# Kernel optimization log

Hardware: AMD Instinct MI355X
Metric: run time of the kernel (lower is better)

## Reference

```python
import jax, jax.numpy as jnp
import numpy as np
import math

B, S, E, R = 128, 16, 512, 500  # batch, seq_len, emb_size, relation_num


def setup_inputs() -> dict:
    key = jax.random.key(0)
    ks = jax.random.split(key, 12)
    s = 1.0 / math.sqrt(E)
    emb = jax.random.normal(ks[0], (R + 1, E), jnp.float32) * s
    emb = emb.at[R].set(0.0)  # padding_idx row is zero in torch
    w_ih = jax.random.normal(ks[1], (4 * E, E), jnp.float32) * s
    w_hh = jax.random.normal(ks[2], (4 * E, E), jnp.float32) * s
    b_ih = jax.random.normal(ks[3], (4 * E,), jnp.float32) * s
    b_hh = jax.random.normal(ks[4], (4 * E,), jnp.float32) * s
    fc_w = jax.random.normal(ks[5], (1, E), jnp.float32) * s
    fc_b = jax.random.normal(ks[6], (1,), jnp.float32) * s
    fcq_w = jax.random.normal(ks[7], (E, E), jnp.float32) * s
    fcq_b = jax.random.normal(ks[8], (E,), jnp.float32) * s
    fck_w = jax.random.normal(ks[9], (E, E), jnp.float32) * s
    fck_b = jax.random.normal(ks[10], (E,), jnp.float32) * s
    tokens = jax.random.randint(ks[11], (B, S), 0, R)  # avoid padding idx R
    return dict(tokens=tokens, emb=emb, w_ih=w_ih, w_hh=w_hh, b_ih=b_ih,
                b_hh=b_hh, fc_w=fc_w, fc_b=fc_b, fcq_w=fcq_w, fcq_b=fcq_b,
                fck_w=fck_w, fck_b=fck_b)


def _lstm_pair(x, w_ih, w_hh, b):
    # x: [..., 2, E]; 2-step LSTM from zero state, return final hidden [..., E]
    def cell(xt, h, c):
        g = xt @ w_ih.T + h @ w_hh.T + b
        i, f, gg, o = jnp.split(g, 4, axis=-1)  # torch gate order i,f,g,o
        c = jax.nn.sigmoid(f) * c + jax.nn.sigmoid(i) * jnp.tanh(gg)
        return jax.nn.sigmoid(o) * jnp.tanh(c), c
    z = jnp.zeros_like(x[..., 0, :])
    h1, c1 = cell(x[..., 0, :], z, z)
    h2, _ = cell(x[..., 1, :], h1, c1)
    return h2


def _attention(x, rel_emb, fcq_w, fcq_b, fck_w, fck_b):
    # x: [B,q,E]; keys = [relation embeddings ; x] -> scores [B,q,R+q]
    b = x.shape[0]
    rel = jnp.broadcast_to(rel_emb[None], (b,) + rel_emb.shape)
    kin = jnp.concatenate([rel, x], axis=1)
    k = kin @ fck_w.T + fck_b
    q = x @ fcq_w.T + fcq_b
    return jnp.einsum('bqe,bke->bqk', q, k) / math.sqrt(E)


def _entropy(scores):
    lp = jax.nn.log_softmax(scores, axis=-1)
    return -jnp.sum(jnp.exp(lp) * lp, axis=-1)


def reference(tokens, emb, w_ih, w_hh, b_ih, b_hh, fc_w, fc_b,
              fcq_w, fcq_b, fck_w, fck_b):
    b_lstm = b_ih + b_hh
    rel_emb = emb[:R]  # relation embeddings used as attention keys/values
    cur = emb[tokens]  # [B,S,E]
    bidx = jnp.arange(B)
    losses = []
    for L in range(S, 1, -1):  # lengths processed: S, S-1, ..., 2
        if L > 2:
            # all adjacent pairs, batched 2-step LSTM: [B, L-1, E]
            pairs = jnp.stack([cur[:, :-1], cur[:, 1:]], axis=2)
            h = _lstm_pair(pairs, w_ih, w_hh, b_lstm)
            sc = jax.nn.sigmoid(h @ fc_w.T + fc_b)[..., 0]  # [B, L-1]
            sel = jnp.argmax(sc, axis=-1)  # [B]
            selected = jnp.take_along_axis(h, sel[:, None, None], axis=1)  # [B,1,E]
            scores = _attention(selected, rel_emb, fcq_w, fcq_b, fck_w, fck_b)
            losses.append(_entropy(scores))  # [B,1]
            # weightedAverage: mask is all-False for seq_len==1, plain softmax
            prob = jax.nn.softmax(scores, axis=-1)  # [B,1,R+1]
            all_emb = jnp.concatenate(
                [jnp.broadcast_to(rel_emb[None], (B, R, E)), selected], axis=1)
            merged = jnp.einsum('bqk,bke->bqe', prob, all_emb)[:, 0]  # [B,E]
            # output = inputs.detach().clone(); write merged at sel; drop row sel+1
            base = jax.lax.stop_gradient(cur)
            base = base.at[bidx, sel].set(merged)
            j = jnp.arange(L - 1)[None, :]
            src = j + (j > sel[:, None]).astype(j.dtype)
            cur = jnp.take_along_axis(base, src[:, :, None], axis=1)  # [B,L-1,E]
        else:  # L == 2: plain LSTM over the two tokens
            h = _lstm_pair(cur, w_ih, w_hh, b_lstm)  # [B,E]
            cur = h[:, None, :]
            losses.append(jnp.zeros((B, 1), cur.dtype))
    scores_f = _attention(cur, rel_emb, fcq_w, fcq_b, fck_w, fck_b)  # [B,1,R+1]
    losses.append(_entropy(scores_f))
    loss_tensor = jnp.concatenate(losses, axis=-1)  # [B,S]
    return scores_f[:, 0], loss_tensor
```

## Files before the change

### kernel.cpp

```cpp
#include <hip/hip_runtime.h>
#include <hip/hip_bf16.h>

#define BB 128
#define SS 16
#define EE 512
#define RR 500
#define G4 2048
#define OUT0 64128
#define NSC 501
#define NPAIR 2047
#define NSU 1012

__device__ __forceinline__ float sigm(float x) { return 1.f / (1.f + expf(-x)); }

__device__ float g_blstm[G4];
__device__ float g_blstmr[G4];
__device__ float g_wihr[G4 * EE];
__device__ float g_whhr[G4 * EE];
__device__ float g_fcw[EE + 4];
__device__ float g_qbias[1024];
__device__ float g_Krel[RR * EE];
__device__ float g_cur[BB * SS * EE];
__device__ float g_G[BB * SS * G4];
__device__ float g_h1[BB * SS * EE];
__device__ float g_c1[BB * SS * EE];
__device__ float g_h2[BB * SS * EE];
__device__ float g_sc[BB * SS];
__device__ float g_ent[BB * SS];
__device__ int   g_sel[BB];
__device__ int   g_ord[BB * SS];
__device__ float g_fckwT[EE * EE];
__device__ float g_fcqwT[EE * EE];
__device__ float g_W2[RR * EE];
__device__ float g_Mx[EE * EE];
__device__ float g_c2[RR + 4];
__device__ float g_v1[EE];
__device__ float g_c0[1];
__device__ float g_su[BB * NSU];

__global__ void k_prep(const float* __restrict__ bih, const float* __restrict__ bhh,
                       const float* __restrict__ fcwv, const float* __restrict__ fcbv,
                       const float* __restrict__ fcqb, const float* __restrict__ fckb) {
    int i = blockIdx.x * blockDim.x + threadIdx.x;
    if (i < G4) g_blstm[i] = bih[i] + bhh[i];
    if (i < EE) {
        g_fcw[i] = fcwv[i];
        g_qbias[i] = fcqb[i];
        g_qbias[EE + i] = fckb[i];
    }
    if (i == 0) g_fcw[EE] = fcbv[0];
    if (i < BB * SS) g_ord[i] = i;
}

__global__ void k_reord(const float* __restrict__ wih, const float* __restrict__ whh) {
    int i = blockIdx.x * blockDim.x + threadIdx.x;
    if (i >= G4 * EE) return;
    int n = i >> 9;
    int k = i & (EE - 1);
    int e = n & (EE - 1);
    int gate = n >> 9;
    int np = 4 * e + gate;
    g_wihr[(size_t)np * EE + k] = wih[i];
    g_whhr[(size_t)np * EE + k] = whh[i];
    if (k == 0) g_blstmr[np] = g_blstm[n];
}

__global__ void k_gather(const int* __restrict__ tok, const float* __restrict__ emb) {
    int i = blockIdx.x * blockDim.x + threadIdx.x;
    if (i >= BB * SS * EE) return;
    int e = i & (EE - 1);
    int r = i >> 9;
    int t = tok[r];
    g_cur[i] = emb[(size_t)t * EE + e];
}

__global__ void k_tr(const float* __restrict__ fckw, const float* __restrict__ fcqw) {
    int i = blockIdx.x * blockDim.x + threadIdx.x;
    if (i >= EE * EE) return;
    int ep = i >> 9;
    int f = i & (EE - 1);
    g_fckwT[(size_t)f * EE + ep] = fckw[(size_t)ep * EE + f];
    g_fcqwT[(size_t)f * EE + ep] = fcqw[(size_t)ep * EE + f];
}

__global__ __launch_bounds__(512) void k_vprep(const float* __restrict__ fcqw, const float* __restrict__ fckw) {
    __shared__ float sh[512];
    int t = threadIdx.x;
    int blk = blockIdx.x;
    if (blk == 0) {
        float acc = 0.f;
        for (int ep = 0; ep < EE; ep++)
            acc += g_qbias[ep] * fckw[(size_t)ep * EE + t] + g_qbias[EE + ep] * fcqw[(size_t)ep * EE + t];
        g_v1[t] = acc;
    } else if (blk == 1) {
        sh[t] = g_qbias[t] * g_qbias[EE + t];
        __syncthreads();
        for (int s = 256; s > 0; s >>= 1) { if (t < s) sh[t] += sh[t + s]; __syncthreads(); }
        if (t == 0) g_c0[0] = sh[0];
    } else {
        int k = blk - 2;
        sh[t] = g_Krel[(size_t)k * EE + t] * g_qbias[t];
        __syncthreads();
        for (int s = 256; s > 0; s >>= 1) { if (t < s) sh[t] += sh[t + s]; __syncthreads(); }
        if (t == 0) g_c2[k] = sh[0];
    }
}

#define TM 32
#define TN 64
#define TK 32
__device__ __forceinline__ void gemm_dev(
    const float* __restrict__ A, int lda,
    const float* __restrict__ W, int ldw,
    const float* __restrict__ bias, const float* __restrict__ Dadd, int ldd,
    float* __restrict__ C, int ldc, int M, int N, int K)
{
    __shared__ __align__(16) float As[2][TK][TM + 2];
    __shared__ __align__(16) float Ws[2][TK][TN + 4];
    int tid = threadIdx.x;
    int mt = blockIdx.y * TM;
    int nt = blockIdx.x * TN;
    int tr = tid >> 4;
    int tc = tid & 15;
    float acc[2][4] = {{0.f,0.f,0.f,0.f},{0.f,0.f,0.f,0.f}};

    int ea = tid * 4;
    int ra = ea >> 5;
    int ka = ea & 31;
    int gmA = mt + ra;
    bool rokA = gmA < M;
    const float* Arow = A + (size_t)(rokA ? gmA : 0) * lda;
    int ew = tid * 8;
    int rw = ew >> 5;
    int kw = ew & 31;
    int gnW = nt + rw;
    bool rokW = gnW < N;
    const float* Wrow = W + (size_t)(rokW ? gnW : 0) * ldw;

    float4 pa = {0,0,0,0}, pw0 = {0,0,0,0}, pw1 = {0,0,0,0};
    if (rokA) pa = *(const float4*)&Arow[ka];
    if (rokW) { pw0 = *(const float4*)&Wrow[kw]; pw1 = *(const float4*)&Wrow[kw + 4]; }
    As[0][ka + 0][ra] = pa.x; As[0][ka + 1][ra] = pa.y; As[0][ka + 2][ra] = pa.z; As[0][ka + 3][ra] = pa.w;
    Ws[0][kw + 0][rw] = pw0.x; Ws[0][kw + 1][rw] = pw0.y; Ws[0][kw + 2][rw] = pw0.z; Ws[0][kw + 3][rw] = pw0.w;
    Ws[0][kw + 4][rw] = pw1.x; Ws[0][kw + 5][rw] = pw1.y; Ws[0][kw + 6][rw] = pw1.z; Ws[0][kw + 7][rw] = pw1.w;
    __syncthreads();

    int P = K / TK;
    for (int p = 0; p < P; p++) {
        int cur = p & 1;
        bool more = (p + 1) < P;
        if (more) {
            int k2 = (p + 1) * TK;
            if (rokA) pa = *(const float4*)&Arow[k2 + ka];
            if (rokW) { pw0 = *(const float4*)&Wrow[k2 + kw]; pw1 = *(const float4*)&Wrow[k2 + kw + 4]; }
        }
        #pragma unroll
        for (int kk = 0; kk < TK; kk++) {
            const float2 a = *(const float2*)&As[cur][kk][2 * tr];
            const float4 w = *(const float4*)&Ws[cur][kk][4 * tc];
            acc[0][0] += a.x * w.x; acc[0][1] += a.x * w.y; acc[0][2] += a.x * w.z; acc[0][3] += a.x * w.w;
            acc[1][0] += a.y * w.x; acc[1][1] += a.y * w.y; acc[1][2] += a.y * w.z; acc[1][3] += a.y * w.w;
        }
        if (more) {
            int nxt = cur ^ 1;
            As[nxt][ka + 0][ra] = pa.x; As[nxt][ka + 1][ra] = pa.y; As[nxt][ka + 2][ra] = pa.z; As[nxt][ka + 3][ra] = pa.w;
            Ws[nxt][kw + 0][rw] = pw0.x; Ws[nxt][kw + 1][rw] = pw0.y; Ws[nxt][kw + 2][rw] = pw0.z; Ws[nxt][kw + 3][rw] = pw0.w;
            Ws[nxt][kw + 4][rw] = pw1.x; Ws[nxt][kw + 5][rw] = pw1.y; Ws[nxt][kw + 6][rw] = pw1.z; Ws[nxt][kw + 7][rw] = pw1.w;
        }
        __syncthreads();
    }
    #pragma unroll
    for (int i = 0; i < 2; i++) {
        int gm = mt + 2 * tr + i;
        if (gm >= M) continue;
        #pragma unroll
        for (int j = 0; j < 4; j++) {
            int gn = nt + 4 * tc + j;
            if (gn >= N) continue;
            float v = (i == 0) ? ((j == 0) ? acc[0][0] : (j == 1) ? acc[0][1] : (j == 2) ? acc[0][2] : acc[0][3])
                               : ((j == 0) ? acc[1][0] : (j == 1) ? acc[1][1] : (j == 2) ? acc[1][2] : acc[1][3]);
            if (bias) v += bias[gn];
            if (Dadd) v += Dadd[(size_t)gm * ldd + gn];
            C[(size_t)gm * ldc + gn] = v;
        }
    }
}

#define UM 128
#define UN 64
#define UK 32
template<int MODE>
__global__ __launch_bounds__(256) void kg_bigF() {
    __shared__ __align__(16) float As[UK][UM + 4];
    __shared__ __align__(16) float Ws[UK][UN + 4];
    const float* __restrict__ A = (MODE == 0) ? g_cur : g_h1;
    const float* __restrict__ W = (MODE == 0) ? g_wihr : g_whhr;
    const int M = (MODE == 0) ? (BB * SS) : NPAIR;
    int tid = threadIdx.x;
    int mt = blockIdx.y * UM;
    int nt = blockIdx.x * UN;
    int tr = tid >> 4;
    int tc = tid & 15;
    float acc[8][4] = {};

    int ra = tid & 127;
    int ka = (tid >> 7) << 4;
    int gmA = mt + ra;
    bool rokA = gmA < M;
    const float* Arow = A + (size_t)(rokA ? gmA : 0) * EE;
    int rw = tid & 63;
    int kw = (tid >> 6) << 3;
    const float* Wrow = W + (size_t)(nt + rw) * EE;

    float4 pa[4] = {};
    float4 pw[2];
    #pragma unroll
    for (int j = 0; j < 4; j++) if (rokA) pa[j] = *(const float4*)&Arow[ka + 4 * j];
    #pragma unroll
    for (int j = 0; j < 2; j++) pw[j] = *(const float4*)&Wrow[kw + 4 * j];

    for (int kt = 0; kt < EE; kt += UK) {
        #pragma unroll
        for (int j = 0; j < 4; j++) {
            As[ka + 4 * j + 0][ra] = pa[j].x;
            As[ka + 4 * j + 1][ra] = pa[j].y;
            As[ka + 4 * j + 2][ra] = pa[j].z;
            As[ka + 4 * j + 3][ra] = pa[j].w;
        }
        #pragma unroll
        for (int j = 0; j < 2; j++) {
            Ws[kw + 4 * j + 0][rw] = pw[j].x;
            Ws[kw + 4 * j + 1][rw] = pw[j].y;
            Ws[kw + 4 * j + 2][rw] = pw[j].z;
            Ws[kw + 4 * j + 3][rw] = pw[j].w;
        }
        __syncthreads();
        if (kt + UK < EE) {
            int k2 = kt + UK;
            #pragma unroll
            for (int j = 0; j < 4; j++) if (rokA) pa[j] = *(const float4*)&Arow[k2 + ka + 4 * j];
            #pragma unroll
            for (int j = 0; j < 2; j++) pw[j] = *(const float4*)&Wrow[k2 + kw + 4 * j];
        }
        #pragma unroll
        for (int kk = 0; kk < UK; kk++) {
            const float4 aA = *(const float4*)&As[kk][4 * tr];
            const float4 aB = *(const float4*)&As[kk][64 + 4 * tr];
            const float4 w4 = *(const float4*)&Ws[kk][4 * tc];
            const float am[8] = {aA.x, aA.y, aA.z, aA.w, aB.x, aB.y, aB.z, aB.w};
            const float wn[4] = {w4.x, w4.y, w4.z, w4.w};
            #pragma unroll
            for (int i = 0; i < 8; i++)
                #pragma unroll
                for (int j = 0; j < 4; j++)
                    acc[i][j] += am[i] * wn[j];
        }
        __syncthreads();
    }

    int c0 = nt + 4 * tc;
    int e0 = (nt >> 2) + tc;
    #pragma unroll
    for (int ri = 0; ri < 8; ri++) {
        int row = (ri < 4) ? (4 * tr + ri) : (60 + 4 * tr + ri);
        int gm = mt + row;
        if (gm >= M) continue;
        float qx = acc[ri][0], qy = acc[ri][1], qz = acc[ri][2], qw = acc[ri][3];
        if (MODE == 0) {
            const float4 b4 = *(const float4*)&g_blstmr[c0];
            qx += b4.x; qy += b4.y; qz += b4.z; qw += b4.w;
            float4 o = {qx, qy, qz, qw};
            *(float4*)&g_G[(size_t)gm * G4 + c0] = o;
            float cA = sigm(qx) * tanhf(qz);
            g_c1[(size_t)gm * EE + e0] = cA;
            g_h1[(size_t)gm * EE + e0] = sigm(qw) * tanhf(cA);
        } else {
            const float4 d4 = *(const float4*)&g_G[(size_t)(gm + 1) * G4 + c0];
            qx += d4.x; qy += d4.y; qz += d4.z; qw += d4.w;
            float c1v = g_c1[(size_t)gm * EE + e0];
            float cA = sigm(qy) * c1v + sigm(qx) * tanhf(qz);
            g_h2[(size_t)gm * EE + e0] = sigm(qw) * tanhf(cA);
        }
    }
}

__global__ __launch_bounds__(256) void kg_Krel(const float* __restrict__ emb, const float* __restrict__ fckw) {
    gemm_dev(emb, EE, fckw, EE, g_qbias + EE, nullptr, 0, g_Krel, EE, RR, EE, EE);
}
__global__ __launch_bounds__(256) void kg_W2() {
    gemm_dev(g_Krel, EE, g_fcqwT, EE, nullptr, nullptr, 0, g_W2, EE, RR, EE, EE);
}
__global__ __launch_bounds__(256) void kg_Mx() {
    gemm_dev(g_fckwT, EE, g_fcqwT, EE, nullptr, nullptr, 0, g_Mx, EE, EE, EE, EE);
}

__global__ __launch_bounds__(256) void k_scI() {
    int m = blockIdx.x;
    int t = threadIdx.x;
    __shared__ float red[256];
    const float* h = g_h2 + (size_t)m * EE;
    float part = h[t] * g_fcw[t] + h[t + 256] * g_fcw[t + 256];
    red[t] = part;
    __syncthreads();
    for (int s = 128; s > 0; s >>= 1) { if (t < s) red[t] += red[t + s]; __syncthreads(); }
    if (t == 0) g_sc[m] = red[0];
}

__global__ __launch_bounds__(256) void k_scP(int L) {
    int m = blockIdx.x;
    int b = m >> 1;
    int tcand = m & 1;
    int s = g_sel[b];
    int p = s - 1 + tcand;
    bool valid = tcand == 0 ? (s >= 1) : (s <= L - 3);
    if (!valid) return;
    int physL = g_ord[b * SS + p];
    int t = threadIdx.x;
    __shared__ float red[256];
    const float* h = g_h2 + (size_t)physL * EE;
    float part = h[t] * g_fcw[t] + h[t + 256] * g_fcw[t + 256];
    red[t] = part;
    __syncthreads();
    for (int s2 = 128; s2 > 0; s2 >>= 1) { if (t < s2) red[t] += red[t + s2]; __syncthreads(); }
    if (t == 0) g_sc[b * SS + p] = red[0];
}

__global__ __launch_bounds__(256) void kg_su(int P) {
    __shared__ __align__(16) float As[2][TK][TM + 2];
    __shared__ __align__(16) float Ws[2][TK][TN + 4];
    __shared__ int s_phys[TM];
    int tid = threadIdx.x;
    int mt = blockIdx.y * TM;
    int nt = blockIdx.x * TN;
    int tr = tid >> 4;
    int tc = tid & 15;
    float acc[2][4] = {{0.f,0.f,0.f,0.f},{0.f,0.f,0.f,0.f}};

    if (tid < TM) {
        int b = mt + tid;
        float best = -1e30f; int bi = 0;
        for (int p = 0; p < P; p++) {
            float v = g_sc[b * SS + p];
            if (v > best) { best = v; bi = p; }
        }
        s_phys[tid] = g_ord[b * SS + bi];
        if (blockIdx.x == 0) g_sel[b] = bi;
    }
    __syncthreads();

    int ea = tid * 4;
    int ra = ea >> 5;
    int ka = ea & 31;
    const float* Arow = g_h2 + (size_t)s_phys[ra] * EE;
    int ew = tid * 8;
    int rw = ew >> 5;
    int kw = ew & 31;
    int gnW = nt + rw;
    bool rokW = gnW < NSU;
    const float* Wrow = nullptr;
    if (rokW) Wrow = (gnW < RR) ? (g_W2 + (size_t)gnW * EE) : (g_Mx + (size_t)(gnW - RR) * EE);

    float4 pa = *(const float4*)&Arow[ka];
    float4 pw0 = {0,0,0,0}, pw1 = {0,0,0,0};
    if (rokW) { pw0 = *(const float4*)&Wrow[kw]; pw1 = *(const float4*)&Wrow[kw + 4]; }
    As[0][ka + 0][ra] = pa.x; As[0][ka + 1][ra] = pa.y; As[0][ka + 2][ra] = pa.z; As[0][ka + 3][ra] = pa.w;
    Ws[0][kw + 0][rw] = pw0.x; Ws[0][kw + 1][rw] = pw0.y; Ws[0][kw + 2][rw] = pw0.z; Ws[0][kw + 3][rw] = pw0.w;
    Ws[0][kw + 4][rw] = pw1.x; Ws[0][kw + 5][rw] = pw1.y; Ws[0][kw + 6][rw] = pw1.z; Ws[0][kw + 7][rw] = pw1.w;
    __syncthreads();

    const int NP = EE / TK;
    for (int p = 0; p < NP; p++) {
        int cur = p & 1;
        bool more = (p + 1) < NP;
        if (more) {
            int k2 = (p + 1) * TK;
            pa = *(const float4*)&Arow[k2 + ka];
            if (rokW) { pw0 = *(const float4*)&Wrow[k2 + kw]; pw1 = *(const float4*)&Wrow[k2 + kw + 4]; }
        }
        #pragma unroll
        for (int kk = 0; kk < TK; kk++) {
            const float2 a = *(const float2*)&As[cur][kk][2 * tr];
            const float4 w = *(const float4*)&Ws[cur][kk][4 * tc];
            acc[0][0] += a.x * w.x; acc[0][1] += a.x * w.y; acc[0][2] += a.x * w.z; acc[0][3] += a.x * w.w;
            acc[1][0] += a.y * w.x; acc[1][1] += a.y * w.y; acc[1][2] += a.y * w.z; acc[1][3] += a.y * w.w;
        }
        if (more) {
            int nxt = cur ^ 1;
            As[nxt][ka + 0][ra] = pa.x; As[nxt][ka + 1][ra] = pa.y; As[nxt][ka + 2][ra] = pa.z; As[nxt][ka + 3][ra] = pa.w;
            Ws[nxt][kw + 0][rw] = pw0.x; Ws[nxt][kw + 1][rw] = pw0.y; Ws[nxt][kw + 2][rw] = pw0.z; Ws[nxt][kw + 3][rw] = pw0.w;
            Ws[nxt][kw + 4][rw] = pw1.x; Ws[nxt][kw + 5][rw] = pw1.y; Ws[nxt][kw + 6][rw] = pw1.z; Ws[nxt][kw + 7][rw] = pw1.w;
        }
        __syncthreads();
    }
    #pragma unroll
    for (int i = 0; i < 2; i++) {
        int gm = mt + 2 * tr + i;
        #pragma unroll
        for (int j = 0; j < 4; j++) {
            int gn = nt + 4 * tc + j;
            if (gn >= NSU) continue;
            float v = (i == 0) ? ((j == 0) ? acc[0][0] : (j == 1) ? acc[0][1] : (j == 2) ? acc[0][2] : acc[0][3])
                               : ((j == 0) ? acc[1][0] : (j == 1) ? acc[1][1] : (j == 2) ? acc[1][2] : acc[1][3]);
            g_su[(size_t)gm * NSU + gn] = v + (gn < RR ? g_c2[gn] : 0.f);
        }
    }
}

__global__ __launch_bounds__(256) void kg_GiF() {
    __shared__ __align__(16) float As[2][TK][TM + 2];
    __shared__ __align__(16) float Ws[2][TK][TN + 4];
    __shared__ int s_phys[TM];
    int tid = threadIdx.x;
    int mt = blockIdx.y * TM;
    int nt = blockIdx.x * TN;
    int tr = tid >> 4;
    int tc = tid & 15;
    float acc[2][4] = {{0.f,0.f,0.f,0.f},{0.f,0.f,0.f,0.f}};

    if (tid < TM) {
        int b = mt + tid;
        s_phys[tid] = g_ord[b * SS + g_sel[b]];
    }
    __syncthreads();

    int ea = tid * 4;
    int ra = ea >> 5;
    int ka = ea & 31;
    const float* Arow = g_cur + (size_t)s_phys[ra] * EE;
    int ew = tid * 8;
    int rw = ew >> 5;
    int kw = ew & 31;
    const float* Wrow = g_wihr + (size_t)(nt + rw) * EE;

    float4 pa = *(const float4*)&Arow[ka];
    float4 pw0 = *(const float4*)&Wrow[kw];
    float4 pw1 = *(const float4*)&Wrow[kw + 4];
    As[0][ka + 0][ra] = pa.x; As[0][ka + 1][ra] = pa.y; As[0][ka + 2][ra] = pa.z; As[0][ka + 3][ra] = pa.w;
    Ws[0][kw + 0][rw] = pw0.x; Ws[0][kw + 1][rw] = pw0.y; Ws[0][kw + 2][rw] = pw0.z; Ws[0][kw + 3][rw] = pw0.w;
    Ws[0][kw + 4][rw] = pw1.x; Ws[0][kw + 5][rw] = pw1.y; Ws[0][kw + 6][rw] = pw1.z; Ws[0][kw + 7][rw] = pw1.w;
    __syncthreads();

    const int NP = EE / TK;
    for (int p = 0; p < NP; p++) {
        int cur = p & 1;
        bool more = (p + 1) < NP;
        if (more) {
            int k2 = (p + 1) * TK;
            pa = *(const float4*)&Arow[k2 + ka];
            pw0 = *(const float4*)&Wrow[k2 + kw];
            pw1 = *(const float4*)&Wrow[k2 + kw + 4];
        }
        #pragma unroll
        for (int kk = 0; kk < TK; kk++) {
            const float2 a = *(const float2*)&As[cur][kk][2 * tr];
            const float4 w = *(const float4*)&Ws[cur][kk][4 * tc];
            acc[0][0] += a.x * w.x; acc[0][1] += a.x * w.y; acc[0][2] += a.x * w.z; acc[0][3] += a.x * w.w;
            acc[1][0] += a.y * w.x; acc[1][1] += a.y * w.y; acc[1][2] += a.y * w.z; acc[1][3] += a.y * w.w;
        }
        if (more) {
            int nxt = cur ^ 1;
            As[nxt][ka + 0][ra] = pa.x; As[nxt][ka + 1][ra] = pa.y; As[nxt][ka + 2][ra] = pa.z; As[nxt][ka + 3][ra] = pa.w;
            Ws[nxt][kw + 0][rw] = pw0.x; Ws[nxt][kw + 1][rw] = pw0.y; Ws[nxt][kw + 2][rw] = pw0.z; Ws[nxt][kw + 3][rw] = pw0.w;
            Ws[nxt][kw + 4][rw] = pw1.x; Ws[nxt][kw + 5][rw] = pw1.y; Ws[nxt][kw + 6][rw] = pw1.z; Ws[nxt][kw + 7][rw] = pw1.w;
        }
        __syncthreads();
    }
    int c0 = nt + 4 * tc;
    int e0 = (nt >> 2) + tc;
    const float4 b4 = *(const float4*)&g_blstmr[c0];
    #pragma unroll
    for (int i = 0; i < 2; i++) {
        int phys = s_phys[2 * tr + i];
        float qx = acc[i][0] + b4.x;
        float qy = acc[i][1] + b4.y;
        float qz = acc[i][2] + b4.z;
        float qw = acc[i][3] + b4.w;
        float4 o = {qx, qy, qz, qw};
        *(float4*)&g_G[(size_t)phys * G4 + c0] = o;
        float cA = sigm(qx) * tanhf(qz);
        g_c1[(size_t)phys * EE + e0] = cA;
        g_h1[(size_t)phys * EE + e0] = sigm(qw) * tanhf(cA);
    }
}

__global__ __launch_bounds__(256) void kg_g2iF(int L) {
    __shared__ __align__(16) float As[2][TK][TM + 2];
    __shared__ __align__(16) float Ws[2][TK][TN + 4];
    __shared__ int s_physA[TM];
    __shared__ int s_physD[TM];
    __shared__ int s_val[TM];
    int tid = threadIdx.x;
    int mt = blockIdx.y * TM;
    int nt = blockIdx.x * TN;
    int tr = tid >> 4;
    int tc = tid & 15;
    float acc[2][4] = {{0.f,0.f,0.f,0.f},{0.f,0.f,0.f,0.f}};

    if (tid < TM) {
        int gm = mt + tid;
        int b = gm >> 1;
        int tcand = gm & 1;
        int s = g_sel[b];
        int p = min(max(s - 1 + tcand, 0), 14);
        s_physA[tid] = g_ord[b * SS + p];
        s_physD[tid] = g_ord[b * SS + p + 1];
        s_val[tid] = tcand == 0 ? (s >= 1) : (s <= L - 3);
    }
    __syncthreads();

    int ea = tid * 4;
    int ra = ea >> 5;
    int ka = ea & 31;
    const float* Arow = g_h1 + (size_t)s_physA[ra] * EE;
    int ew = tid * 8;
    int rw = ew >> 5;
    int kw = ew & 31;
    const float* Wrow = g_whhr + (size_t)(nt + rw) * EE;

    float4 pa = *(const float4*)&Arow[ka];
    float4 pw0 = *(const float4*)&Wrow[kw];
    float4 pw1 = *(const float4*)&Wrow[kw + 4];
    As[0][ka + 0][ra] = pa.x; As[0][ka + 1][ra] = pa.y; As[0][ka + 2][ra] = pa.z; As[0][ka + 3][ra] = pa.w;
    Ws[0][kw + 0][rw] = pw0.x; Ws[0][kw + 1][rw] = pw0.y; Ws[0][kw + 2][rw] = pw0.z; Ws[0][kw + 3][rw] = pw0.w;
    Ws[0][kw + 4][rw] = pw1.x; Ws[0][kw + 5][rw] = pw1.y; Ws[0][kw + 6][rw] = pw1.z; Ws[0][kw + 7][rw] = pw1.w;
    __syncthreads();

    const int NP = EE / TK;
    for (int p = 0; p < NP; p++) {
        int cur = p & 1;
        bool more = (p + 1) < NP;
        if (more) {
            int k2 = (p + 1) * TK;
            pa = *(const float4*)&Arow[k2 + ka];
            pw0 = *(const float4*)&Wrow[k2 + kw];
            pw1 = *(const float4*)&Wrow[k2 + kw + 4];
        }
        #pragma unroll
        for (int kk = 0; kk < TK; kk++) {
            const float2 a = *(const float2*)&As[cur][kk][2 * tr];
            const float4 w = *(const float4*)&Ws[cur][kk][4 * tc];
            acc[0][0] += a.x * w.x; acc[0][1] += a.x * w.y; acc[0][2] += a.x * w.z; acc[0][3] += a.x * w.w;
            acc[1][0] += a.y * w.x; acc[1][1] += a.y * w.y; acc[1][2] += a.y * w.z; acc[1][3] += a.y * w.w;
        }
        if (more) {
            int nxt = cur ^ 1;
            As[nxt][ka + 0][ra] = pa.x; As[nxt][ka + 1][ra] = pa.y; As[nxt][ka + 2][ra] = pa.z; As[nxt][ka + 3][ra] = pa.w;
            Ws[nxt][kw + 0][rw] = pw0.x; Ws[nxt][kw + 1][rw] = pw0.y; Ws[nxt][kw + 2][rw] = pw0.z; Ws[nxt][kw + 3][rw] = pw0.w;
            Ws[nxt][kw + 4][rw] = pw1.x; Ws[nxt][kw + 5][rw] = pw1.y; Ws[nxt][kw + 6][rw] = pw1.z; Ws[nxt][kw + 7][rw] = pw1.w;
        }
        __syncthreads();
    }
    int c0 = nt + 4 * tc;
    int e0 = (nt >> 2) + tc;
    #pragma unroll
    for (int i = 0; i < 2; i++) {
        int r = 2 * tr + i;
        if (!s_val[r]) continue;
        int pA = s_physA[r];
        int pD = s_physD[r];
        const float4 d4 = *(const float4*)&g_G[(size_t)pD * G4 + c0];
        float qx = acc[i][0] + d4.x;
        float qy = acc[i][1] + d4.y;
        float qz = acc[i][2] + d4.z;
        float qw = acc[i][3] + d4.w;
        float c1v = g_c1[(size_t)pA * EE + e0];
        float cA = sigm(qy) * c1v + sigm(qx) * tanhf(qz);
        g_h2[(size_t)pA * EE + e0] = sigm(qw) * tanhf(cA);
    }
}

__global__ __launch_bounds__(512) void k_smu(int col, int finalFlag, int L,
                                             const float* __restrict__ emb, float* __restrict__ out) {
    int b = blockIdx.x;
    int t = threadIdx.x;
    __shared__ float sh[512];
    __shared__ float srow[NSC];
    __shared__ float s_p500;
    const float* su = g_su + (size_t)b * NSU;
    int s = g_sel[b];
    int phys = g_ord[b * SS + s];
    const float* h2row = g_h2 + (size_t)phys * EE;
    const float isq = 0.044194173824159216f;

    float hv = h2row[t];
    sh[t] = hv * (su[RR + t] + g_v1[t]);
    __syncthreads();
    for (int ss = 256; ss > 0; ss >>= 1) { if (t < ss) sh[t] += sh[t + ss]; __syncthreads(); }
    if (t == 0) srow[RR] = (sh[0] + g_c0[0]) * isq;
    __syncthreads();
    if (t < RR) srow[t] = su[t] * isq;
    __syncthreads();
    float mx = (t < NSC) ? srow[t] : -1e30f;
    sh[t] = mx; __syncthreads();
    for (int ss = 256; ss > 0; ss >>= 1) { if (t < ss) sh[t] = fmaxf(sh[t], sh[t + ss]); __syncthreads(); }
    mx = sh[0]; __syncthreads();
    float zp = (t < NSC) ? expf(srow[t] - mx) : 0.f;
    sh[t] = zp; __syncthreads();
    for (int ss = 256; ss > 0; ss >>= 1) { if (t < ss) sh[t] += sh[t + ss]; __syncthreads(); }
    float lse = mx + logf(sh[0]);
    __syncthreads();
    float pb = (t < NSC) ? expf(srow[t] - lse) : 0.f;
    float ep = (t < NSC) ? pb * (lse - srow[t]) : 0.f;
    if (finalFlag && t < NSC) out[(size_t)b * NSC + t] = srow[t];
    sh[t] = ep; __syncthreads();
    for (int ss = 256; ss > 0; ss >>= 1) { if (t < ss) sh[t] += sh[t + ss]; __syncthreads(); }
    if (finalFlag) {
        if (t < 16) {
            float v = (t == 15) ? sh[0] : ((t == 14) ? 0.f : g_ent[b * SS + t]);
            out[OUT0 + b * 16 + t] = v;
        }
        return;
    }
    if (t == 0) g_ent[b * SS + col] = sh[0];

    __syncthreads();
    if (t < NSC) srow[t] = pb;
    if (t == RR) s_p500 = pb;
    __syncthreads();
    float macc = 0.f;
    #pragma unroll 4
    for (int k = 0; k < RR; k++) macc += srow[k] * emb[(size_t)k * EE + t];
    g_cur[(size_t)phys * EE + t] = macc + s_p500 * hv;
    if (t == 0) {
        for (int j = s + 1; j <= L - 2; j++) g_ord[b * SS + j] = g_ord[b * SS + j + 1];
        for (int pp = s + 1; pp <= L - 3; pp++) g_sc[b * SS + pp] = g_sc[b * SS + pp + 1];
    }
}

extern "C" void kernel_launch(void* const* d_in, const int* in_sizes, int n_in,
                              void* d_out, int out_size, void* d_ws, size_t ws_size,
                              hipStream_t stream) {
    const int*   tokens = (const int*)d_in[0];
    const float* emb    = (const float*)d_in[1];
    const float* wih    = (const float*)d_in[2];
    const float* whh    = (const float*)d_in[3];
    const float* bih    = (const float*)d_in[4];
    const float* bhh    = (const float*)d_in[5];
    const float* fcwv   = (const float*)d_in[6];
    const float* fcbv   = (const float*)d_in[7];
    const float* fcqw   = (const float*)d_in[8];
    const float* fcqb   = (const float*)d_in[9];
    const float* fckw   = (const float*)d_in[10];
    const float* fckb   = (const float*)d_in[11];
    float* out = (float*)d_out;

    auto grid32 = [](int M, int N) { return dim3((unsigned)((N + TN - 1) / TN), (unsigned)((M + TM - 1) / TM)); };

    k_prep<<<dim3(8), dim3(256), 0, stream>>>(bih, bhh, fcwv, fcbv, fcqb, fckb);
    k_reord<<<dim3((G4 * EE) / 256), dim3(256), 0, stream>>>(wih, whh);
    kg_Krel<<<grid32(RR, EE), dim3(256), 0, stream>>>(emb, fckw);
    k_tr<<<dim3((EE * EE + 255) / 256), dim3(256), 0, stream>>>(fckw, fcqw);
    kg_W2<<<grid32(RR, EE), dim3(256), 0, stream>>>();
    kg_Mx<<<grid32(EE, EE), dim3(256), 0, stream>>>();
    k_vprep<<<dim3(502), dim3(512), 0, stream>>>(fcqw, fckw);
    k_gather<<<dim3((BB * SS * EE + 255) / 256), dim3(256), 0, stream>>>(tokens, emb);

    kg_bigF<0><<<dim3(32, 16), dim3(256), 0, stream>>>();
    kg_bigF<1><<<dim3(32, 16), dim3(256), 0, stream>>>();
    k_scI<<<dim3(NPAIR), dim3(256), 0, stream>>>();

    for (int L = SS; L >= 3; L--) {
        kg_su<<<grid32(BB, NSU), dim3(256), 0, stream>>>(L - 1);
        k_smu<<<dim3(BB), dim3(512), 0, stream>>>(SS - L, 0, L, emb, out);
        kg_GiF<<<grid32(BB, G4), dim3(256), 0, stream>>>();
        kg_g2iF<<<grid32(2 * BB, G4), dim3(256), 0, stream>>>(L);
        k_scP<<<dim3(2 * BB), dim3(256), 0, stream>>>(L);
    }

    kg_su<<<grid32(BB, NSU), dim3(256), 0, stream>>>(1);
    k_smu<<<dim3(BB), dim3(512), 0, stream>>>(15, 1, 2, emb, out);

    (void)in_sizes; (void)n_in; (void)out_size; (void)d_ws; (void)ws_size;
}
```

Measured before the change: 1.691 ms.

## Fuse pair-score recompute into su GEMM and double-buffer bigF shared tiles

Removes the separate k_scP launch per reduction step. Each kg_suF block now recomputes the two neighbour pair scores itself into a shared score table before the argmax. Because a block reads the previous step's selection while new selections are written, the selection array is ping-ponged by parity. The kg_bigF GEMM also moves to double-buffered shared tiles, so the next tile is stored after compute and one barrier per k-step is dropped. The costs are extra redundant dot products in every su block and twice the shared memory in bigF, which may lower occupancy.

New measurement: 1.854 ms. 9.6% more time.

```diff
diff --git a/kernel.cpp b/kernel.cpp
--- a/kernel.cpp
+++ b/kernel.cpp
@@ -17,7 +17,7 @@
 __device__ float g_blstmr[G4];
 __device__ float g_wihr[G4 * EE];
 __device__ float g_whhr[G4 * EE];
-__device__ float g_fcw[EE + 4];
+__device__ __align__(16) float g_fcw[EE + 4];
 __device__ float g_qbias[1024];
 __device__ float g_Krel[RR * EE];
 __device__ float g_cur[BB * SS * EE];
@@ -27,7 +27,7 @@
 __device__ float g_h2[BB * SS * EE];
 __device__ float g_sc[BB * SS];
 __device__ float g_ent[BB * SS];
-__device__ int   g_sel[BB];
+__device__ int   g_selPP[2 * BB];
 __device__ int   g_ord[BB * SS];
 __device__ float g_fckwT[EE * EE];
 __device__ float g_fcqwT[EE * EE];
@@ -191,8 +191,8 @@
 #define UK 32
 template<int MODE>
 __global__ __launch_bounds__(256) void kg_bigF() {
-    __shared__ __align__(16) float As[UK][UM + 4];
-    __shared__ __align__(16) float Ws[UK][UN + 4];
+    __shared__ __align__(16) float As[2][UK][UM + 4];
+    __shared__ __align__(16) float Ws[2][UK][UN + 4];
     const float* __restrict__ A = (MODE == 0) ? g_cur : g_h1;
     const float* __restrict__ W = (MODE == 0) ? g_wihr : g_whhr;
     const int M = (MODE == 0) ? (BB * SS) : NPAIR;
@@ -218,25 +218,28 @@
     for (int j = 0; j < 4; j++) if (rokA) pa[j] = *(const float4*)&Arow[ka + 4 * j];
     #pragma unroll
     for (int j = 0; j < 2; j++) pw[j] = *(const float4*)&Wrow[kw + 4 * j];
-
-    for (int kt = 0; kt < EE; kt += UK) {
-        #pragma unroll
-        for (int j = 0; j < 4; j++) {
-            As[ka + 4 * j + 0][ra] = pa[j].x;
-            As[ka + 4 * j + 1][ra] = pa[j].y;
-            As[ka + 4 * j + 2][ra] = pa[j].z;
-            As[ka + 4 * j + 3][ra] = pa[j].w;
-        }
-        #pragma unroll
-        for (int j = 0; j < 2; j++) {
-            Ws[kw + 4 * j + 0][rw] = pw[j].x;
-            Ws[kw + 4 * j + 1][rw] = pw[j].y;
-            Ws[kw + 4 * j + 2][rw] = pw[j].z;
-            Ws[kw + 4 * j + 3][rw] = pw[j].w;
-        }
-        __syncthreads();
-        if (kt + UK < EE) {
-            int k2 = kt + UK;
+    #pragma unroll
+    for (int j = 0; j < 4; j++) {
+        As[0][ka + 4 * j + 0][ra] = pa[j].x;
+        As[0][ka + 4 * j + 1][ra] = pa[j].y;
+        As[0][ka + 4 * j + 2][ra] = pa[j].z;
+        As[0][ka + 4 * j + 3][ra] = pa[j].w;
+    }
+    #pragma unroll
+    for (int j = 0; j < 2; j++) {
+        Ws[0][kw + 4 * j + 0][rw] = pw[j].x;
+        Ws[0][kw + 4 * j + 1][rw] = pw[j].y;
+        Ws[0][kw + 4 * j + 2][rw] = pw[j].z;
+        Ws[0][kw + 4 * j + 3][rw] = pw[j].w;
+    }
+    __syncthreads();
+
+    const int NP = EE / UK;
+    for (int p = 0; p < NP; p++) {
+        int cur = p & 1;
+        bool more = (p + 1) < NP;
+        if (more) {
+            int k2 = (p + 1) * UK;
             #pragma unroll
             for (int j = 0; j < 4; j++) if (rokA) pa[j] = *(const float4*)&Arow[k2 + ka + 4 * j];
             #pragma unroll
@@ -244,9 +247,9 @@
         }
         #pragma unroll
         for (int kk = 0; kk < UK; kk++) {
-            const float4 aA = *(const float4*)&As[kk][4 * tr];
-            const float4 aB = *(const float4*)&As[kk][64 + 4 * tr];
-            const float4 w4 = *(const float4*)&Ws[kk][4 * tc];
+            const float4 aA = *(const float4*)&As[cur][kk][4 * tr];
+            const float4 aB = *(const float4*)&As[cur][kk][64 + 4 * tr];
+            const float4 w4 = *(const float4*)&Ws[cur][kk][4 * tc];
             const float am[8] = {aA.x, aA.y, aA.z, aA.w, aB.x, aB.y, aB.z, aB.w};
             const float wn[4] = {w4.x, w4.y, w4.z, w4.w};
             #pragma unroll
@@ -254,6 +257,23 @@
                 #pragma unroll
                 for (int j = 0; j < 4; j++)
                     acc[i][j] += am[i] * wn[j];
+        }
+        if (more) {
+            int nxt = cur ^ 1;
+            #pragma unroll
+            for (int j = 0; j < 4; j++) {
+                As[nxt][ka + 4 * j + 0][ra] = pa[j].x;
+                As[nxt][ka + 4 * j + 1][ra] = pa[j].y;
+                As[nxt][ka + 4 * j + 2][ra] = pa[j].z;
+                As[nxt][ka + 4 * j + 3][ra] = pa[j].w;
+            }
+            #pragma unroll
+            for (int j = 0; j < 2; j++) {
+                Ws[nxt][kw + 4 * j + 0][rw] = pw[j].x;
+                Ws[nxt][kw + 4 * j + 1][rw] = pw[j].y;
+                Ws[nxt][kw + 4 * j + 2][rw] = pw[j].z;
+                Ws[nxt][kw + 4 * j + 3][rw] = pw[j].w;
+            }
         }
         __syncthreads();
     }
@@ -306,29 +326,11 @@
     if (t == 0) g_sc[m] = red[0];
 }
 
-__global__ __launch_bounds__(256) void k_scP(int L) {
-    int m = blockIdx.x;
-    int b = m >> 1;
-    int tcand = m & 1;
-    int s = g_sel[b];
-    int p = s - 1 + tcand;
-    bool valid = tcand == 0 ? (s >= 1) : (s <= L - 3);
-    if (!valid) return;
-    int physL = g_ord[b * SS + p];
-    int t = threadIdx.x;
-    __shared__ float red[256];
-    const float* h = g_h2 + (size_t)physL * EE;
-    float part = h[t] * g_fcw[t] + h[t + 256] * g_fcw[t + 256];
-    red[t] = part;
-    __syncthreads();
-    for (int s2 = 128; s2 > 0; s2 >>= 1) { if (t < s2) red[t] += red[t + s2]; __syncthreads(); }
-    if (t == 0) g_sc[b * SS + p] = red[0];
-}
-
-__global__ __launch_bounds__(256) void kg_su(int P) {
+__global__ __launch_bounds__(256) void kg_suF(int P, int prevL, int firstFlag, int par) {
     __shared__ __align__(16) float As[2][TK][TM + 2];
     __shared__ __align__(16) float Ws[2][TK][TN + 4];
     __shared__ int s_phys[TM];
+    __shared__ float s_scl[TM][SS];
     int tid = threadIdx.x;
     int mt = blockIdx.y * TM;
     int nt = blockIdx.x * TN;
@@ -336,15 +338,49 @@
     int tc = tid & 15;
     float acc[2][4] = {{0.f,0.f,0.f,0.f},{0.f,0.f,0.f,0.f}};
 
+    #pragma unroll
+    for (int u = tid; u < TM * SS; u += 256)
+        s_scl[u >> 4][u & 15] = g_sc[(mt + (u >> 4)) * SS + (u & 15)];
+    __syncthreads();
+
+    if (!firstFlag) {
+        int q = tid >> 2;
+        int sub = tid & 3;
+        int r = q >> 1;
+        int c = q & 1;
+        int b = mt + r;
+        int sp = g_selPP[(par ^ 1) * BB + b];
+        bool valid = (c == 0) ? (sp >= 1) : (sp <= prevL - 3);
+        int p = valid ? (sp - 1 + c) : 0;
+        float sum = 0.f;
+        if (valid) {
+            const float* h = g_h2 + (size_t)g_ord[b * SS + p] * EE + sub * 128;
+            const float* f = g_fcw + sub * 128;
+            #pragma unroll 8
+            for (int j = 0; j < 32; j++) {
+                const float4 hv = *(const float4*)(h + 4 * j);
+                const float4 fv = *(const float4*)(f + 4 * j);
+                sum += hv.x * fv.x + hv.y * fv.y + hv.z * fv.z + hv.w * fv.w;
+            }
+        }
+        sum += __shfl_down(sum, 1, 64);
+        sum += __shfl_down(sum, 2, 64);
+        if (sub == 0 && valid) {
+            s_scl[r][p] = sum;
+            if (blockIdx.x == 0) g_sc[b * SS + p] = sum;
+        }
+    }
+    __syncthreads();
+
     if (tid < TM) {
         int b = mt + tid;
         float best = -1e30f; int bi = 0;
         for (int p = 0; p < P; p++) {
-            float v = g_sc[b * SS + p];
+            float v = s_scl[tid][p];
             if (v > best) { best = v; bi = p; }
         }
         s_phys[tid] = g_ord[b * SS + bi];
-        if (blockIdx.x == 0) g_sel[b] = bi;
+        if (blockIdx.x == 0) g_selPP[par * BB + b] = bi;
     }
     __syncthreads();
 
@@ -406,7 +442,7 @@
     }
 }
 
-__global__ __launch_bounds__(256) void kg_GiF() {
+__global__ __launch_bounds__(256) void kg_GiF(int par) {
     __shared__ __align__(16) float As[2][TK][TM + 2];
     __shared__ __align__(16) float Ws[2][TK][TN + 4];
     __shared__ int s_phys[TM];
@@ -419,7 +455,7 @@
 
     if (tid < TM) {
         int b = mt + tid;
-        s_phys[tid] = g_ord[b * SS + g_sel[b]];
+        s_phys[tid] = g_ord[b * SS + g_selPP[par * BB + b]];
     }
     __syncthreads();
 
@@ -483,7 +519,7 @@
     }
 }
 
-__global__ __launch_bounds__(256) void kg_g2iF(int L) {
+__global__ __launch_bounds__(256) void kg_g2iF(int L, int par) {
     __shared__ __align__(16) float As[2][TK][TM + 2];
     __shared__ __align__(16) float Ws[2][TK][TN + 4];
     __shared__ int s_physA[TM];
@@ -500,7 +536,7 @@
         int gm = mt + tid;
         int b = gm >> 1;
         int tcand = gm & 1;
-        int s = g_sel[b];
+        int s = g_selPP[par * BB + b];
         int p = min(max(s - 1 + tcand, 0), 14);
         s_physA[tid] = g_ord[b * SS + p];
         s_physD[tid] = g_ord[b * SS + p + 1];
@@ -569,7 +605,7 @@
     }
 }
 
-__global__ __launch_bounds__(512) void k_smu(int col, int finalFlag, int L,
+__global__ __launch_bounds__(512) void k_smu(int col, int finalFlag, int L, int par,
                                              const float* __restrict__ emb, float* __restrict__ out) {
     int b = blockIdx.x;
     int t = threadIdx.x;
@@ -577,7 +613,7 @@
     __shared__ float srow[NSC];
     __shared__ float s_p500;
     const float* su = g_su + (size_t)b * NSU;
-    int s = g_sel[b];
+    int s = g_selPP[par * BB + b];
     int phys = g_ord[b * SS + s];
     const float* h2row = g_h2 + (size_t)phys * EE;
     const float isq = 0.044194173824159216f;
@@ -660,15 +696,15 @@
     k_scI<<<dim3(NPAIR), dim3(256), 0, stream>>>();
 
     for (int L = SS; L >= 3; L--) {
-        kg_su<<<grid32(BB, NSU), dim3(256), 0, stream>>>(L - 1);
-        k_smu<<<dim3(BB), dim3(512), 0, stream>>>(SS - L, 0, L, emb, out);
-        kg_GiF<<<grid32(BB, G4), dim3(256), 0, stream>>>();
-        kg_g2iF<<<grid32(2 * BB, G4), dim3(256), 0, stream>>>(L);
-        k_scP<<<dim3(2 * BB), dim3(256), 0, stream>>>(L);
-    }
-
-    kg_su<<<grid32(BB, NSU), dim3(256), 0, stream>>>(1);
-    k_smu<<<dim3(BB), dim3(512), 0, stream>>>(15, 1, 2, emb, out);
+        int par = (SS - L) & 1;
+        kg_suF<<<grid32(BB, NSU), dim3(256), 0, stream>>>(L - 1, L + 1, L == SS ? 1 : 0, par);
+        k_smu<<<dim3(BB), dim3(512), 0, stream>>>(SS - L, 0, L, par, emb, out);
+        kg_GiF<<<grid32(BB, G4), dim3(256), 0, stream>>>(par);
+        kg_g2iF<<<grid32(2 * BB, G4), dim3(256), 0, stream>>>(L, par);
+    }
+
+    kg_suF<<<grid32(BB, NSU), dim3(256), 0, stream>>>(1, 3, 0, 0);
+    k_smu<<<dim3(BB), dim3(512), 0, stream>>>(15, 1, 2, 0, emb, out);
 
     (void)in_sizes; (void)n_in; (void)out_size; (void)d_ws; (void)ws_size;
 }
```
